# Kernel tuning notes

Measured on AMD Instinct MI355X. Metric: run time of the kernel, lower is better.

Reference implementation:

```python
import jax, jax.numpy as jnp
import numpy as np

DIM = 1024
HEADS = 16
DIM_HEAD = 64
INNER = HEADS * DIM_HEAD  # 1024
MAX_POS = 512
B, N = 2, 1024


def setup_inputs() -> dict:
    key = jax.random.key(0)
    ks = jax.random.split(key, 6)
    s = DIM ** -0.5
    x = jax.random.normal(ks[0], (B, N, DIM), dtype=jnp.float32)
    Wq = jax.random.normal(ks[1], (DIM, INNER), dtype=jnp.float32) * s
    Wkv = jax.random.normal(ks[2], (DIM, 2 * INNER), dtype=jnp.float32) * s
    Wo = jax.random.normal(ks[3], (INNER, DIM), dtype=jnp.float32) * (INNER ** -0.5)
    bo = jnp.zeros((DIM,), dtype=jnp.float32)
    rel_emb = jax.random.normal(ks[4], (2 * MAX_POS + 1, DIM_HEAD), dtype=jnp.float32)
    return {"x": x, "Wq": Wq, "Wkv": Wkv, "Wo": Wo, "bo": bo, "rel_emb": rel_emb}


def reference(x, Wq, Wkv, Wo, bo, rel_emb):
    b, n, _ = x.shape
    scale = DIM_HEAD ** -0.5
    q = x @ Wq                    # [b, n, inner]
    kv = x @ Wkv                  # [b, n, 2*inner]
    k, v = jnp.split(kv, 2, axis=-1)

    def split_heads(t):
        return t.reshape(b, n, HEADS, DIM_HEAD).transpose(0, 2, 1, 3)  # [b,h,n,d]

    q, k, v = map(split_heads, (q, k, v))
    dots = jnp.einsum('bhid,bhjd->bhij', q, k) * scale

    seq = jnp.arange(n)
    dist = jnp.clip(seq[:, None] - seq[None, :], -MAX_POS, MAX_POS) + MAX_POS  # [n, n]
    rel = rel_emb[dist]           # [n, n, d]
    pos_attn = jnp.einsum('bhnd,nrd->bhnr', q, rel) * scale
    dots = dots + pos_attn

    attn = jax.nn.softmax(dots, axis=-1)
    out = jnp.einsum('bhij,bhjd->bhid', attn, v)
    out = out.transpose(0, 2, 1, 3).reshape(b, n, INNER)
    return out @ Wo + bo
```

## Files before the change

### kernel.cpp

```cpp
#include <hip/hip_runtime.h>

typedef __bf16 bf16x8 __attribute__((ext_vector_type(8)));
typedef float f32x4 __attribute__((ext_vector_type(4)));

#define DEV __device__ __forceinline__

DEV unsigned short f2bf(float f) {
  union { float f; unsigned u; } x; x.f = f;
  unsigned r = x.u + 0x7FFFu + ((x.u >> 16) & 1u);
  return (unsigned short)(r >> 16);
}
DEV float bf2f(unsigned short h) {
  union { unsigned u; float f; } x; x.u = ((unsigned)h) << 16;
  return x.f;
}
DEV unsigned short bfc(float f) {
  union { __bf16 b; unsigned short u; } c; c.b = (__bf16)f; return c.u;
}

typedef __attribute__((address_space(3))) void* lds_vp;
typedef const __attribute__((address_space(1))) void* gbl_vp;
DEV void load_lds16(const unsigned short* gp, void* lp) {
  __builtin_amdgcn_global_load_lds((gbl_vp)(const void*)gp, (lds_vp)lp, 16, 0, 0);
}

__global__ __launch_bounds__(256)
void prep_k(const float* __restrict__ x, const float* __restrict__ rel,
            const float* __restrict__ bo, const float* __restrict__ Wq,
            const float* __restrict__ Wkv, const float* __restrict__ Wo,
            unsigned short* __restrict__ xb, unsigned short* __restrict__ relb,
            unsigned short* __restrict__ bob, unsigned short* __restrict__ WqkvT,
            unsigned short* __restrict__ WoT) {
  __shared__ unsigned short tile[32][33];
  const int bid = blockIdx.x, tid = threadIdx.x;
  if (bid < 2114) {
    const float* src; unsigned short* dst; long base; long n;
    if (bid < 2048)      { src = x;   dst = xb;   base = (long)bid * 1024;          n = 2097152; }
    else if (bid < 2113) { src = rel; dst = relb; base = (long)(bid - 2048) * 1024; n = 65600; }
    else                 { src = bo;  dst = bob;  base = 0;                          n = 1024; }
    long i = base + tid * 4;
    if (i < n) {
      float4 v = *(const float4*)&src[i];
      unsigned long long u = (unsigned long long)f2bf(v.x)
                           | ((unsigned long long)f2bf(v.y) << 16)
                           | ((unsigned long long)f2bf(v.z) << 32)
                           | ((unsigned long long)f2bf(v.w) << 48);
      *(unsigned long long*)&dst[i] = u;
    }
  } else {
    int id = bid - 2114;
    const float* src; unsigned short* dst; const int R = 1024; int C, txt, tyt;
    if (id < 1024)      { src = Wq;  dst = WqkvT;           C = 1024; txt = id & 31; tyt = id >> 5; }
    else if (id < 3072) { int l = id - 1024; src = Wkv; dst = WqkvT + 1048576; C = 2048; txt = l & 63; tyt = l >> 6; }
    else                { int l = id - 3072; src = Wo;  dst = WoT;             C = 1024; txt = l & 31; tyt = l >> 5; }
    int c0 = txt * 32, r0 = tyt * 32;
    int tx = tid & 31, ty = tid >> 5;
    #pragma unroll
    for (int i = 0; i < 4; ++i)
      tile[ty + i * 8][tx] = f2bf(src[(size_t)(r0 + ty + i * 8) * C + c0 + tx]);
    __syncthreads();
    #pragma unroll
    for (int i = 0; i < 4; ++i)
      dst[(size_t)(c0 + ty + i * 8) * R + r0 + tx] = tile[tx][ty + i * 8];
  }
}

DEV void stage16(const unsigned short* gbase, size_t gstride,
                 unsigned short* lbase, int r0, int lane) {
  #pragma unroll
  for (int t = 0; t < 2; ++t) {
    int r = r0 + t * 8 + (lane >> 3);
    int lc = (lane & 7) ^ (r & 7);
    load_lds16(&gbase[(size_t)r * gstride + lc * 8], &lbase[(size_t)(r0 + t * 8) * 64]);
  }
}
DEV bf16x8 read_swz(const unsigned short* buf, int row, int lc) {
  int pc = lc ^ (row & 7);
  return *(const bf16x8*)&buf[row * 64 + pc * 8];
}

__global__ __launch_bounds__(256)
void gemm_qkv(const unsigned short* __restrict__ A,
              const unsigned short* __restrict__ Bt,
              unsigned short* __restrict__ o0,
              unsigned short* __restrict__ o1,
              unsigned short* __restrict__ o2) {
  __shared__ __align__(16) unsigned short As[64 * 64];
  __shared__ __align__(16) unsigned short Bs[128 * 64];
  __shared__ unsigned short tbuf[64][68];
  const int tid  = threadIdx.x;
  const int lane = tid & 63, wave = tid >> 6;
  const int q15  = lane & 15, quad = lane >> 4;
  const int wr = wave >> 1, wc = wave & 1;
  const int m0 = blockIdx.y * 64, n0 = blockIdx.x * 128;
  const int K = 1024;

  f32x4 acc[2][4] = {};
  for (int k0 = 0; k0 < K; k0 += 64) {
    __syncthreads();
    stage16(&A[(size_t)m0 * K + k0], K, As, wave * 16, lane);
    stage16(&Bt[(size_t)n0 * K + k0], K, Bs, wave * 32, lane);
    stage16(&Bt[(size_t)n0 * K + k0], K, Bs, wave * 32 + 16, lane);
    __syncthreads();
    #pragma unroll
    for (int ks = 0; ks < 2; ++ks) {
      bf16x8 af[2], bfr[4];
      #pragma unroll
      for (int i = 0; i < 2; ++i)
        af[i] = read_swz(As, wr * 32 + i * 16 + q15, ks * 4 + quad);
      #pragma unroll
      for (int j = 0; j < 4; ++j)
        bfr[j] = read_swz(Bs, wc * 64 + j * 16 + q15, ks * 4 + quad);
      #pragma unroll
      for (int i = 0; i < 2; ++i)
        #pragma unroll
        for (int j = 0; j < 4; ++j)
          acc[i][j] = __builtin_amdgcn_mfma_f32_16x16x32_bf16(af[i], bfr[j], acc[i][j], 0, 0, 0);
    }
  }

  const int b = m0 >> 10, nn0 = m0 & 1023;
  if (n0 < 2048) {
    #pragma unroll
    for (int i = 0; i < 2; ++i)
      #pragma unroll
      for (int j = 0; j < 4; ++j)
        #pragma unroll
        for (int r = 0; r < 4; ++r) {
          int row = m0 + wr * 32 + i * 16 + quad * 4 + r;
          int col = n0 + wc * 64 + j * 16 + q15;
          float v = acc[i][j][r];
          int nn = row & 1023;
          unsigned short* dst; int c = col; float sc = 1.f;
          if (col < 1024) { dst = o0; sc = 0.125f; }
          else            { dst = o1; c = col - 1024; }
          int h = c >> 6, dd = c & 63;
          dst[((size_t)((row >> 10) * 16 + h) * 1024 + nn) * 64 + dd] = f2bf(v * sc);
        }
  } else {
    const int hp = (n0 - 2048) >> 6;
    #pragma unroll
    for (int hh = 0; hh < 2; ++hh) {
      __syncthreads();
      if (wc == hh) {
        #pragma unroll
        for (int i = 0; i < 2; ++i)
          #pragma unroll
          for (int j = 0; j < 4; ++j)
            #pragma unroll
            for (int r = 0; r < 4; ++r)
              tbuf[wr * 32 + i * 16 + quad * 4 + r][j * 16 + q15] = f2bf(acc[i][j][r]);
      }
      __syncthreads();
      const int bh = b * 16 + hp + hh;
      const int d = tid >> 2, nb = (tid & 3) * 16;
      #pragma unroll
      for (int s = 0; s < 2; ++s) {
        int n = nb + s * 8;
        union { uint4 v; unsigned short us[8]; } t;
        #pragma unroll
        for (int e = 0; e < 8; ++e) t.us[e] = tbuf[n + e][d];
        *(uint4*)&o2[((size_t)bh * 64 + d) * 1024 + nn0 + n] = t.v;
      }
    }
  }
}

__global__ __launch_bounds__(512)
void flash_attn(const unsigned short* __restrict__ q_ws,
                const unsigned short* __restrict__ k_ws,
                const unsigned short* __restrict__ vt_ws,
                const unsigned short* __restrict__ rel,
                unsigned short* __restrict__ ao) {
  __shared__ __align__(16) unsigned short Kbuf[2][64 * 64];
  __shared__ __align__(16) unsigned short Vbuf[2][64 * 64];
  __shared__ __align__(16) unsigned short P_lds[8][16 * 64];
  union TXu {
    unsigned short T[8][16][84];
    float bnc[4][65][17];
  };
  __shared__ __align__(16) TXu tx;

  const int tid  = threadIdx.x;
  const int lane = tid & 63, w = tid >> 6;
  const int q15  = lane & 15, quad = lane >> 4;
  const int wr4  = w & 3, jh = w >> 2;
  const int bh = blockIdx.x;
  const int ib = blockIdx.y * 64 + wr4 * 16;

  const unsigned short* qp = q_ws  + (size_t)bh * 1024 * 64;
  const unsigned short* kp = k_ws  + (size_t)bh * 1024 * 64;
  const unsigned short* tp = vt_ws + (size_t)bh * 64 * 1024;

  unsigned short* Kb = &Kbuf[jh][0];
  unsigned short* Vb = &Vbuf[jh][0];
  unsigned short* Trow = &tx.T[w][q15][0];
  unsigned short* Prow = &P_lds[w][q15 * 64];

  bf16x8 aq[2];
  #pragma unroll
  for (int ks = 0; ks < 2; ++ks)
    aq[ks] = *(const bf16x8*)&qp[(size_t)(ib + q15) * 64 + ks * 32 + quad * 8];

  f32x4 o[4] = {};
  float l_acc = 0.f;

  for (int jt = 0; jt < 8; ++jt) {
    const int j0 = jh * 512 + jt * 64;
    __syncthreads();
    stage16(kp + (size_t)j0 * 64, 64, Kb, wr4 * 16, lane);
    stage16(tp + j0, 1024, Vb, wr4 * 16, lane);

    int tb = ib - j0 + 512 - 63;
    f32x4 accT[5] = {};
    #pragma unroll
    for (int ks = 0; ks < 2; ++ks)
      #pragma unroll
      for (int ub = 0; ub < 5; ++ub) {
        int trow = tb + ub * 16 + q15;
        trow = trow < 0 ? 0 : (trow > 1024 ? 1024 : trow);
        bf16x8 br = *(const bf16x8*)&rel[(size_t)trow * 64 + ks * 32 + quad * 8];
        accT[ub] = __builtin_amdgcn_mfma_f32_16x16x32_bf16(br, aq[ks], accT[ub], 0, 0, 0);
      }
    #pragma unroll
    for (int ub = 0; ub < 5; ++ub) {
      uint2 tw;
      tw.x = (unsigned)bfc(accT[ub][0]) | ((unsigned)bfc(accT[ub][1]) << 16);
      tw.y = (unsigned)bfc(accT[ub][2]) | ((unsigned)bfc(accT[ub][3]) << 16);
      *(uint2*)&Trow[ub * 16 + quad * 4] = tw;
    }

    __syncthreads();

    f32x4 accS[4] = {};
    #pragma unroll
    for (int ks = 0; ks < 2; ++ks)
      #pragma unroll
      for (int cb = 0; cb < 4; ++cb) {
        bf16x8 bk = read_swz(Kb, cb * 16 + q15, ks * 4 + quad);
        accS[cb] = __builtin_amdgcn_mfma_f32_16x16x32_bf16(bk, aq[ks], accS[cb], 0, 0, 0);
      }

    #pragma unroll
    for (int cb = 0; cb < 4; ++cb) {
      float p[4];
      #pragma unroll
      for (int r = 0; r < 4; ++r) {
        int jl = cb * 16 + quad * 4 + r;
        float s = accS[cb][r] + bf2f(Trow[63 + q15 - jl]);
        p[r] = exp2f(fmaf(s, 1.44269504f, -64.f));
        l_acc += p[r];
      }
      uint2 pw;
      pw.x = (unsigned)bfc(p[0]) | ((unsigned)bfc(p[1]) << 16);
      pw.y = (unsigned)bfc(p[2]) | ((unsigned)bfc(p[3]) << 16);
      int phys = (cb * 2 + (quad >> 1)) ^ (q15 & 7);
      *(uint2*)&Prow[phys * 8 + (quad & 1) * 4] = pw;
    }

    #pragma unroll
    for (int ks = 0; ks < 2; ++ks) {
      bf16x8 ap = *(const bf16x8*)&Prow[(((ks * 4 + quad) ^ (q15 & 7))) * 8];
      #pragma unroll
      for (int db = 0; db < 4; ++db) {
        bf16x8 bv = read_swz(Vb, db * 16 + q15, ks * 4 + quad);
        o[db] = __builtin_amdgcn_mfma_f32_16x16x32_bf16(bv, ap, o[db], 0, 0, 0);
      }
    }
  }

  l_acc += __shfl_xor(l_acc, 16, 64);
  l_acc += __shfl_xor(l_acc, 32, 64);

  __syncthreads();

  if (w >= 4) {
    const int ww = w - 4;
    #pragma unroll
    for (int db = 0; db < 4; ++db)
      #pragma unroll
      for (int r = 0; r < 4; ++r)
        tx.bnc[ww][db * 16 + quad * 4 + r][q15] = o[db][r];
    tx.bnc[ww][64][q15] = l_acc;
  }
  __syncthreads();
  if (w < 4) {
    float lB = tx.bnc[w][64][q15];
    float inv = 1.f / (l_acc + lB + 1e-30f);
    unsigned short* Bt = (unsigned short*)&Kbuf[0][0] + (size_t)w * 16 * 72;
    #pragma unroll
    for (int db = 0; db < 4; ++db) {
      float v0 = (o[db][0] + tx.bnc[w][db * 16 + quad * 4 + 0][q15]) * inv;
      float v1 = (o[db][1] + tx.bnc[w][db * 16 + quad * 4 + 1][q15]) * inv;
      float v2 = (o[db][2] + tx.bnc[w][db * 16 + quad * 4 + 2][q15]) * inv;
      float v3 = (o[db][3] + tx.bnc[w][db * 16 + quad * 4 + 3][q15]) * inv;
      uint2 bw;
      bw.x = (unsigned)bfc(v0) | ((unsigned)bfc(v1) << 16);
      bw.y = (unsigned)bfc(v2) | ((unsigned)bfc(v3) << 16);
      *(uint2*)&Bt[q15 * 72 + db * 16 + quad * 4] = bw;
    }
    const int il = lane >> 2, ch = (lane & 3) * 16;
    bf16x8 u0 = *(const bf16x8*)&Bt[il * 72 + ch];
    bf16x8 u1 = *(const bf16x8*)&Bt[il * 72 + ch + 8];
    const int b = bh >> 4, h = bh & 15;
    size_t addr = ((size_t)(b * 1024 + blockIdx.y * 64 + w * 16 + il)) * 1024
                + h * 64 + ch;
    *(bf16x8*)&ao[addr] = u0;
    *(bf16x8*)&ao[addr + 8] = u1;
  }
}

__global__ __launch_bounds__(256)
void gemm_out(const unsigned short* __restrict__ A,
              const unsigned short* __restrict__ Bt,
              const unsigned short* __restrict__ bias,
              float* __restrict__ fo) {
  __shared__ __align__(16) unsigned short As[64 * 64];
  __shared__ __align__(16) unsigned short Bs[64 * 64];
  const int tid  = threadIdx.x;
  const int lane = tid & 63, w = tid >> 6;
  const int q15  = lane & 15, quad = lane >> 4;
  const int m0 = blockIdx.y * 64, n0 = blockIdx.x * 64;
  const int K = 1024, N = 1024;

  f32x4 acc[4] = {};
  for (int k0 = 0; k0 < K; k0 += 64) {
    __syncthreads();
    stage16(&A[(size_t)m0 * K + k0], K, As, w * 16, lane);
    stage16(&Bt[(size_t)n0 * K + k0], K, Bs, w * 16, lane);
    __syncthreads();
    #pragma unroll
    for (int ks = 0; ks < 2; ++ks) {
      bf16x8 af = read_swz(As, w * 16 + q15, ks * 4 + quad);
      bf16x8 bfr[4];
      #pragma unroll
      for (int j = 0; j < 4; ++j)
        bfr[j] = read_swz(Bs, j * 16 + q15, ks * 4 + quad);
      #pragma unroll
      for (int j = 0; j < 4; ++j)
        acc[j] = __builtin_amdgcn_mfma_f32_16x16x32_bf16(af, bfr[j], acc[j], 0, 0, 0);
    }
  }
  #pragma unroll
  for (int j = 0; j < 4; ++j)
    #pragma unroll
    for (int r = 0; r < 4; ++r) {
      int row = m0 + w * 16 + quad * 4 + r;
      int col = n0 + j * 16 + q15;
      fo[(size_t)row * N + col] = acc[j][r] + bf2f(bias[col]);
    }
}

extern "C" void kernel_launch(void* const* d_in, const int* in_sizes, int n_in,
                              void* d_out, int out_size, void* d_ws, size_t ws_size,
                              hipStream_t stream) {
  (void)in_sizes; (void)n_in; (void)out_size; (void)ws_size;
  const float* x   = (const float*)d_in[0];
  const float* Wq  = (const float*)d_in[1];
  const float* Wkv = (const float*)d_in[2];
  const float* Wo  = (const float*)d_in[3];
  const float* bo  = (const float*)d_in[4];
  const float* rel = (const float*)d_in[5];
  float* out = (float*)d_out;

  unsigned short* ws = (unsigned short*)d_ws;
  unsigned short* WoT   = ws;
  unsigned short* relb  = WoT   + 1048576;
  unsigned short* bob   = relb  + 65664;
  unsigned short* q_ws  = bob   + 1088;
  unsigned short* k_ws  = q_ws  + 2097152;
  unsigned short* vT    = k_ws  + 2097152;
  unsigned short* WqkvT = vT    + 2097152;
  unsigned short* xb    = WqkvT + 3145728;
  unsigned short* ao    = WqkvT;

  prep_k<<<6210, 256, 0, stream>>>(x, rel, bo, Wq, Wkv, Wo,
                                   xb, relb, bob, WqkvT, WoT);
  gemm_qkv<<<dim3(24, 32), 256, 0, stream>>>(xb, WqkvT, q_ws, k_ws, vT);
  flash_attn<<<dim3(32, 16), 512, 0, stream>>>(q_ws, k_ws, vT, relb, ao);
  gemm_out<<<dim3(16, 32), 256, 0, stream>>>(ao, WoT, bob, out);
}
```

Baseline: 157.8 us.

## Restructure flash attention to 4 waves with double-buffered K/V and rel prefetch

Each block now runs 4 waves, and each wave walks all 16 key tiles itself. Before, 8 waves split the keys into two halves and merged partial outputs through LDS at the end. K and V^T tiles are double-buffered: the next tile is staged while the current one is computed. The rel-embedding rows for the next tile are prefetched into registers. This removes the cross-wave combine and one barrier per iteration, in exchange for half as many resident waves and a longer serial loop per wave. It relies on a plain s_barrier rather than __syncthreads, so correct ordering of the async LDS loads depends on the waitcnt the compiler inserts.

```diff
diff --git a/kernel.cpp b/kernel.cpp
--- a/kernel.cpp
+++ b/kernel.cpp
@@ -166,7 +166,7 @@
   }
 }
 
-__global__ __launch_bounds__(512)
+__global__ __launch_bounds__(256)
 void flash_attn(const unsigned short* __restrict__ q_ws,
                 const unsigned short* __restrict__ k_ws,
                 const unsigned short* __restrict__ vt_ws,
@@ -174,27 +174,20 @@
                 unsigned short* __restrict__ ao) {
   __shared__ __align__(16) unsigned short Kbuf[2][64 * 64];
   __shared__ __align__(16) unsigned short Vbuf[2][64 * 64];
-  __shared__ __align__(16) unsigned short P_lds[8][16 * 64];
-  union TXu {
-    unsigned short T[8][16][84];
-    float bnc[4][65][17];
-  };
-  __shared__ __align__(16) TXu tx;
+  __shared__ __align__(16) unsigned short P_lds[4][16 * 64];
+  __shared__ __align__(16) unsigned short T_lds[4][16][84];
 
   const int tid  = threadIdx.x;
   const int lane = tid & 63, w = tid >> 6;
   const int q15  = lane & 15, quad = lane >> 4;
-  const int wr4  = w & 3, jh = w >> 2;
   const int bh = blockIdx.x;
-  const int ib = blockIdx.y * 64 + wr4 * 16;
+  const int ib = blockIdx.y * 64 + w * 16;
 
   const unsigned short* qp = q_ws  + (size_t)bh * 1024 * 64;
   const unsigned short* kp = k_ws  + (size_t)bh * 1024 * 64;
   const unsigned short* tp = vt_ws + (size_t)bh * 64 * 1024;
 
-  unsigned short* Kb = &Kbuf[jh][0];
-  unsigned short* Vb = &Vbuf[jh][0];
-  unsigned short* Trow = &tx.T[w][q15][0];
+  unsigned short* Trow = &T_lds[w][q15][0];
   unsigned short* Prow = &P_lds[w][q15 * 64];
 
   bf16x8 aq[2];
@@ -205,23 +198,35 @@
   f32x4 o[4] = {};
   float l_acc = 0.f;
 
-  for (int jt = 0; jt < 8; ++jt) {
-    const int j0 = jh * 512 + jt * 64;
-    __syncthreads();
-    stage16(kp + (size_t)j0 * 64, 64, Kb, wr4 * 16, lane);
-    stage16(tp + j0, 1024, Vb, wr4 * 16, lane);
-
-    int tb = ib - j0 + 512 - 63;
-    f32x4 accT[5] = {};
+  stage16(kp, 64, &Kbuf[0][0], w * 16, lane);
+  stage16(tp, 1024, &Vbuf[0][0], w * 16, lane);
+  bf16x8 rr[2][5];
+  {
+    const int tb = ib + 512 - 63;
     #pragma unroll
     for (int ks = 0; ks < 2; ++ks)
       #pragma unroll
       for (int ub = 0; ub < 5; ++ub) {
         int trow = tb + ub * 16 + q15;
         trow = trow < 0 ? 0 : (trow > 1024 ? 1024 : trow);
-        bf16x8 br = *(const bf16x8*)&rel[(size_t)trow * 64 + ks * 32 + quad * 8];
-        accT[ub] = __builtin_amdgcn_mfma_f32_16x16x32_bf16(br, aq[ks], accT[ub], 0, 0, 0);
-      }
+        rr[ks][ub] = *(const bf16x8*)&rel[(size_t)trow * 64 + ks * 32 + quad * 8];
+      }
+  }
+
+  for (int jt = 0; jt < 16; ++jt) {
+    const int j0 = jt * 64, cur = jt & 1;
+    __builtin_amdgcn_s_barrier();
+    if (jt + 1 < 16) {
+      stage16(kp + (size_t)(j0 + 64) * 64, 64, &Kbuf[cur ^ 1][0], w * 16, lane);
+      stage16(tp + (j0 + 64), 1024, &Vbuf[cur ^ 1][0], w * 16, lane);
+    }
+
+    f32x4 accT[5] = {};
+    #pragma unroll
+    for (int ks = 0; ks < 2; ++ks)
+      #pragma unroll
+      for (int ub = 0; ub < 5; ++ub)
+        accT[ub] = __builtin_amdgcn_mfma_f32_16x16x32_bf16(rr[ks][ub], aq[ks], accT[ub], 0, 0, 0);
     #pragma unroll
     for (int ub = 0; ub < 5; ++ub) {
       uint2 tw;
@@ -230,14 +235,26 @@
       *(uint2*)&Trow[ub * 16 + quad * 4] = tw;
     }
 
-    __syncthreads();
+    if (jt + 1 < 16) {
+      const int tb = ib - (j0 + 64) + 512 - 63;
+      #pragma unroll
+      for (int ks = 0; ks < 2; ++ks)
+        #pragma unroll
+        for (int ub = 0; ub < 5; ++ub) {
+          int trow = tb + ub * 16 + q15;
+          trow = trow < 0 ? 0 : (trow > 1024 ? 1024 : trow);
+          rr[ks][ub] = *(const bf16x8*)&rel[(size_t)trow * 64 + ks * 32 + quad * 8];
+        }
+    }
+
+    __builtin_amdgcn_sched_barrier(0);
 
     f32x4 accS[4] = {};
     #pragma unroll
     for (int ks = 0; ks < 2; ++ks)
       #pragma unroll
       for (int cb = 0; cb < 4; ++cb) {
-        bf16x8 bk = read_swz(Kb, cb * 16 + q15, ks * 4 + quad);
+        bf16x8 bk = read_swz(&Kbuf[cur][0], cb * 16 + q15, ks * 4 + quad);
         accS[cb] = __builtin_amdgcn_mfma_f32_16x16x32_bf16(bk, aq[ks], accS[cb], 0, 0, 0);
       }
 
@@ -263,7 +280,7 @@
       bf16x8 ap = *(const bf16x8*)&Prow[(((ks * 4 + quad) ^ (q15 & 7))) * 8];
       #pragma unroll
       for (int db = 0; db < 4; ++db) {
-        bf16x8 bv = read_swz(Vb, db * 16 + q15, ks * 4 + quad);
+        bf16x8 bv = read_swz(&Vbuf[cur][0], db * 16 + q15, ks * 4 + quad);
         o[db] = __builtin_amdgcn_mfma_f32_16x16x32_bf16(bv, ap, o[db], 0, 0, 0);
       }
     }
@@ -271,43 +288,24 @@
 
   l_acc += __shfl_xor(l_acc, 16, 64);
   l_acc += __shfl_xor(l_acc, 32, 64);
-
-  __syncthreads();
-
-  if (w >= 4) {
-    const int ww = w - 4;
-    #pragma unroll
-    for (int db = 0; db < 4; ++db)
-      #pragma unroll
-      for (int r = 0; r < 4; ++r)
-        tx.bnc[ww][db * 16 + quad * 4 + r][q15] = o[db][r];
-    tx.bnc[ww][64][q15] = l_acc;
-  }
-  __syncthreads();
-  if (w < 4) {
-    float lB = tx.bnc[w][64][q15];
-    float inv = 1.f / (l_acc + lB + 1e-30f);
-    unsigned short* Bt = (unsigned short*)&Kbuf[0][0] + (size_t)w * 16 * 72;
-    #pragma unroll
-    for (int db = 0; db < 4; ++db) {
-      float v0 = (o[db][0] + tx.bnc[w][db * 16 + quad * 4 + 0][q15]) * inv;
-      float v1 = (o[db][1] + tx.bnc[w][db * 16 + quad * 4 + 1][q15]) * inv;
-      float v2 = (o[db][2] + tx.bnc[w][db * 16 + quad * 4 + 2][q15]) * inv;
-      float v3 = (o[db][3] + tx.bnc[w][db * 16 + quad * 4 + 3][q15]) * inv;
-      uint2 bw;
-      bw.x = (unsigned)bfc(v0) | ((unsigned)bfc(v1) << 16);
-      bw.y = (unsigned)bfc(v2) | ((unsigned)bfc(v3) << 16);
-      *(uint2*)&Bt[q15 * 72 + db * 16 + quad * 4] = bw;
-    }
-    const int il = lane >> 2, ch = (lane & 3) * 16;
-    bf16x8 u0 = *(const bf16x8*)&Bt[il * 72 + ch];
-    bf16x8 u1 = *(const bf16x8*)&Bt[il * 72 + ch + 8];
-    const int b = bh >> 4, h = bh & 15;
-    size_t addr = ((size_t)(b * 1024 + blockIdx.y * 64 + w * 16 + il)) * 1024
-                + h * 64 + ch;
-    *(bf16x8*)&ao[addr] = u0;
-    *(bf16x8*)&ao[addr + 8] = u1;
-  }
+  float inv = 1.f / (l_acc + 1e-30f);
+
+  unsigned short* Bt = &T_lds[w][0][0];
+  #pragma unroll
+  for (int db = 0; db < 4; ++db) {
+    uint2 bw;
+    bw.x = (unsigned)bfc(o[db][0] * inv) | ((unsigned)bfc(o[db][1] * inv) << 16);
+    bw.y = (unsigned)bfc(o[db][2] * inv) | ((unsigned)bfc(o[db][3] * inv) << 16);
+    *(uint2*)&Bt[q15 * 72 + db * 16 + quad * 4] = bw;
+  }
+  const int il = lane >> 2, ch = (lane & 3) * 16;
+  bf16x8 u0 = *(const bf16x8*)&Bt[il * 72 + ch];
+  bf16x8 u1 = *(const bf16x8*)&Bt[il * 72 + ch + 8];
+  const int b = bh >> 4, h = bh & 15;
+  size_t addr = ((size_t)(b * 1024 + blockIdx.y * 64 + w * 16 + il)) * 1024
+              + h * 64 + ch;
+  *(bf16x8*)&ao[addr] = u0;
+  *(bf16x8*)&ao[addr + 8] = u1;
 }
 
 __global__ __launch_bounds__(256)
@@ -377,6 +375,6 @@
   prep_k<<<6210, 256, 0, stream>>>(x, rel, bo, Wq, Wkv, Wo,
                                    xb, relb, bob, WqkvT, WoT);
   gemm_qkv<<<dim3(24, 32), 256, 0, stream>>>(xb, WqkvT, q_ws, k_ws, vT);
-  flash_attn<<<dim3(32, 16), 512, 0, stream>>>(q_ws, k_ws, vT, relb, ao);
+  flash_attn<<<dim3(32, 16), 256, 0, stream>>>(q_ws, k_ws, vT, relb, ao);
   gemm_out<<<dim3(16, 32), 256, 0, stream>>>(ao, WoT, bob, out);
 }
```

New measurement: 161.0 us. 2.1% more time.

## Enlarge GEMM block tiles and vectorize V-transpose epilogue through LDS

Applied to the files above, without the earlier changes.

The QKV projection GEMM tile grows from 64x128 to 128x128, so each wave now computes a 64x64 sub-tile. The output-projection GEMM tile grows from 64x64 to 64x128 with a 2x2 wave layout. Both changes raise data reuse per staged tile and cut global traffic, but they halve the block counts to 384 and 256, which may underfill the GPU's compute units. The V-transpose epilogue now writes packed 4-element words into a transposed LDS buffer and reads whole rows as uint4 for global stores, replacing the scalar gathers.

```diff
diff --git a/kernel.cpp b/kernel.cpp
--- a/kernel.cpp
+++ b/kernel.cpp
@@ -85,34 +85,35 @@
               unsigned short* __restrict__ o0,
               unsigned short* __restrict__ o1,
               unsigned short* __restrict__ o2) {
-  __shared__ __align__(16) unsigned short As[64 * 64];
+  __shared__ __align__(16) unsigned short As[128 * 64];
   __shared__ __align__(16) unsigned short Bs[128 * 64];
-  __shared__ unsigned short tbuf[64][68];
+  __shared__ __align__(16) unsigned short tbuf[64][136];
   const int tid  = threadIdx.x;
   const int lane = tid & 63, wave = tid >> 6;
   const int q15  = lane & 15, quad = lane >> 4;
   const int wr = wave >> 1, wc = wave & 1;
-  const int m0 = blockIdx.y * 64, n0 = blockIdx.x * 128;
+  const int m0 = blockIdx.y * 128, n0 = blockIdx.x * 128;
   const int K = 1024;
 
-  f32x4 acc[2][4] = {};
+  f32x4 acc[4][4] = {};
   for (int k0 = 0; k0 < K; k0 += 64) {
     __syncthreads();
-    stage16(&A[(size_t)m0 * K + k0], K, As, wave * 16, lane);
+    stage16(&A[(size_t)m0 * K + k0], K, As, wave * 32, lane);
+    stage16(&A[(size_t)m0 * K + k0], K, As, wave * 32 + 16, lane);
     stage16(&Bt[(size_t)n0 * K + k0], K, Bs, wave * 32, lane);
     stage16(&Bt[(size_t)n0 * K + k0], K, Bs, wave * 32 + 16, lane);
     __syncthreads();
     #pragma unroll
     for (int ks = 0; ks < 2; ++ks) {
-      bf16x8 af[2], bfr[4];
-      #pragma unroll
-      for (int i = 0; i < 2; ++i)
-        af[i] = read_swz(As, wr * 32 + i * 16 + q15, ks * 4 + quad);
+      bf16x8 af[4], bfr[4];
+      #pragma unroll
+      for (int i = 0; i < 4; ++i)
+        af[i] = read_swz(As, wr * 64 + i * 16 + q15, ks * 4 + quad);
       #pragma unroll
       for (int j = 0; j < 4; ++j)
         bfr[j] = read_swz(Bs, wc * 64 + j * 16 + q15, ks * 4 + quad);
       #pragma unroll
-      for (int i = 0; i < 2; ++i)
+      for (int i = 0; i < 4; ++i)
         #pragma unroll
         for (int j = 0; j < 4; ++j)
           acc[i][j] = __builtin_amdgcn_mfma_f32_16x16x32_bf16(af[i], bfr[j], acc[i][j], 0, 0, 0);
@@ -122,12 +123,12 @@
   const int b = m0 >> 10, nn0 = m0 & 1023;
   if (n0 < 2048) {
     #pragma unroll
-    for (int i = 0; i < 2; ++i)
+    for (int i = 0; i < 4; ++i)
       #pragma unroll
       for (int j = 0; j < 4; ++j)
         #pragma unroll
         for (int r = 0; r < 4; ++r) {
-          int row = m0 + wr * 32 + i * 16 + quad * 4 + r;
+          int row = m0 + wr * 64 + i * 16 + quad * 4 + r;
           int col = n0 + wc * 64 + j * 16 + q15;
           float v = acc[i][j][r];
           int nn = row & 1023;
@@ -144,23 +145,22 @@
       __syncthreads();
       if (wc == hh) {
         #pragma unroll
-        for (int i = 0; i < 2; ++i)
+        for (int i = 0; i < 4; ++i)
           #pragma unroll
-          for (int j = 0; j < 4; ++j)
-            #pragma unroll
-            for (int r = 0; r < 4; ++r)
-              tbuf[wr * 32 + i * 16 + quad * 4 + r][j * 16 + q15] = f2bf(acc[i][j][r]);
+          for (int j = 0; j < 4; ++j) {
+            uint2 tw;
+            tw.x = (unsigned)f2bf(acc[i][j][0]) | ((unsigned)f2bf(acc[i][j][1]) << 16);
+            tw.y = (unsigned)f2bf(acc[i][j][2]) | ((unsigned)f2bf(acc[i][j][3]) << 16);
+            *(uint2*)&tbuf[j * 16 + q15][wr * 64 + i * 16 + quad * 4] = tw;
+          }
       }
       __syncthreads();
       const int bh = b * 16 + hp + hh;
-      const int d = tid >> 2, nb = (tid & 3) * 16;
-      #pragma unroll
-      for (int s = 0; s < 2; ++s) {
-        int n = nb + s * 8;
-        union { uint4 v; unsigned short us[8]; } t;
-        #pragma unroll
-        for (int e = 0; e < 8; ++e) t.us[e] = tbuf[n + e][d];
-        *(uint4*)&o2[((size_t)bh * 64 + d) * 1024 + nn0 + n] = t.v;
+      const int d = tid >> 2, mc = (tid & 3) * 32;
+      #pragma unroll
+      for (int s = 0; s < 4; ++s) {
+        uint4 t = *(const uint4*)&tbuf[d][mc + s * 8];
+        *(uint4*)&o2[((size_t)bh * 64 + d) * 1024 + nn0 + mc + s * 8] = t;
       }
     }
   }
@@ -316,39 +316,47 @@
               const unsigned short* __restrict__ bias,
               float* __restrict__ fo) {
   __shared__ __align__(16) unsigned short As[64 * 64];
-  __shared__ __align__(16) unsigned short Bs[64 * 64];
+  __shared__ __align__(16) unsigned short Bs[128 * 64];
   const int tid  = threadIdx.x;
   const int lane = tid & 63, w = tid >> 6;
   const int q15  = lane & 15, quad = lane >> 4;
-  const int m0 = blockIdx.y * 64, n0 = blockIdx.x * 64;
+  const int wr = w >> 1, wc = w & 1;
+  const int m0 = blockIdx.y * 64, n0 = blockIdx.x * 128;
   const int K = 1024, N = 1024;
 
-  f32x4 acc[4] = {};
+  f32x4 acc[2][4] = {};
   for (int k0 = 0; k0 < K; k0 += 64) {
     __syncthreads();
     stage16(&A[(size_t)m0 * K + k0], K, As, w * 16, lane);
-    stage16(&Bt[(size_t)n0 * K + k0], K, Bs, w * 16, lane);
+    stage16(&Bt[(size_t)n0 * K + k0], K, Bs, w * 32, lane);
+    stage16(&Bt[(size_t)n0 * K + k0], K, Bs, w * 32 + 16, lane);
     __syncthreads();
     #pragma unroll
     for (int ks = 0; ks < 2; ++ks) {
-      bf16x8 af = read_swz(As, w * 16 + q15, ks * 4 + quad);
-      bf16x8 bfr[4];
+      bf16x8 af[2], bfr[4];
+      #pragma unroll
+      for (int i = 0; i < 2; ++i)
+        af[i] = read_swz(As, wr * 32 + i * 16 + q15, ks * 4 + quad);
       #pragma unroll
       for (int j = 0; j < 4; ++j)
-        bfr[j] = read_swz(Bs, j * 16 + q15, ks * 4 + quad);
-      #pragma unroll
-      for (int j = 0; j < 4; ++j)
-        acc[j] = __builtin_amdgcn_mfma_f32_16x16x32_bf16(af, bfr[j], acc[j], 0, 0, 0);
+        bfr[j] = read_swz(Bs, wc * 64 + j * 16 + q15, ks * 4 + quad);
+      #pragma unroll
+      for (int i = 0; i < 2; ++i)
+        #pragma unroll
+        for (int j = 0; j < 4; ++j)
+          acc[i][j] = __builtin_amdgcn_mfma_f32_16x16x32_bf16(af[i], bfr[j], acc[i][j], 0, 0, 0);
     }
   }
   #pragma unroll
-  for (int j = 0; j < 4; ++j)
-    #pragma unroll
-    for (int r = 0; r < 4; ++r) {
-      int row = m0 + w * 16 + quad * 4 + r;
-      int col = n0 + j * 16 + q15;
-      fo[(size_t)row * N + col] = acc[j][r] + bf2f(bias[col]);
-    }
+  for (int i = 0; i < 2; ++i)
+    #pragma unroll
+    for (int j = 0; j < 4; ++j)
+      #pragma unroll
+      for (int r = 0; r < 4; ++r) {
+        int row = m0 + wr * 32 + i * 16 + quad * 4 + r;
+        int col = n0 + wc * 64 + j * 16 + q15;
+        fo[(size_t)row * N + col] = acc[i][j][r] + bf2f(bias[col]);
+      }
 }
 
 extern "C" void kernel_launch(void* const* d_in, const int* in_sizes, int n_in,
@@ -376,7 +384,7 @@
 
   prep_k<<<6210, 256, 0, stream>>>(x, rel, bo, Wq, Wkv, Wo,
                                    xb, relb, bob, WqkvT, WoT);
-  gemm_qkv<<<dim3(24, 32), 256, 0, stream>>>(xb, WqkvT, q_ws, k_ws, vT);
+  gemm_qkv<<<dim3(24, 16), 256, 0, stream>>>(xb, WqkvT, q_ws, k_ws, vT);
   flash_attn<<<dim3(32, 16), 512, 0, stream>>>(q_ws, k_ws, vT, relb, ao);
-  gemm_out<<<dim3(16, 32), 256, 0, stream>>>(ao, WoT, bob, out);
-}
+  gemm_out<<<dim3(8, 32), 256, 0, stream>>>(ao, WoT, bob, out);
+}
```

New measurement: 164.8 us. +4.4%, slower.
